# Kernel optimization log

Hardware: AMD Instinct MI355X
Metric: run time of the kernel (lower is better)

The kernel has to match this reference:

```python
import jax, jax.numpy as jnp
import numpy as np
from jax import lax

B, C, OUT, K, L = 8, 256, 256, 7, 2048
STRIDE, PAD, DIL = 1, 3, 1

def setup_inputs() -> dict:
    key = jax.random.key(0)
    k1, k2, k3, k4, k5 = jax.random.split(key, 5)
    return {
        "x": jax.random.normal(k1, (B, C, L), jnp.float32),
        "w_off": jax.random.normal(k2, (C * K * 2, C, K), jnp.float32) * 0.02,
        "b_off": jax.random.normal(k3, (C * K * 2,), jnp.float32) * 0.02,
        "weight": jax.random.normal(k4, (OUT, C, K), jnp.float32) * 0.02,
        "bias": jax.random.normal(k5, (OUT,), jnp.float32) * 0.02,
    }

def _gather_lin(x, idx):
    # x: (B,C,Lin), idx: (B,C,K,Lout) -> zero-padded gather along length
    Lin = x.shape[-1]
    valid = (idx >= 0) & (idx < Lin)
    idxc = jnp.clip(idx, 0, Lin - 1)
    v = jnp.take_along_axis(x[:, :, None, :], idxc, axis=3)
    return jnp.where(valid, v, jnp.zeros((), x.dtype))

def reference(x, w_off, b_off, weight, bias):
    # offset/mask predictor conv (same geometry as main conv)
    off = lax.conv_general_dilated(
        x, w_off, window_strides=(STRIDE,), padding=[(PAD, PAD)],
        rhs_dilation=(DIL,), dimension_numbers=("NCH", "OIH", "NCH"))
    off = off + b_off[None, :, None]
    Lout = off.shape[-1]
    off = off.reshape(B, 2, C * K, Lout)
    offset = off[:, 0].reshape(B, C, K, Lout)          # fractional shift per (c,k,p)
    mask = jax.nn.sigmoid(off[:, 1]).reshape(B, C, K, Lout)
    # base sampling grid: p*stride - pad + k*dil
    base = (jnp.arange(Lout) * STRIDE - PAD)[None, :] + (jnp.arange(K) * DIL)[:, None]  # (K,Lout)
    pos = offset + base[None, None].astype(x.dtype)    # (B,C,K,Lout)
    p0 = jnp.floor(pos)
    frac = pos - p0
    p0i = p0.astype(jnp.int32)
    sampled = _gather_lin(x, p0i) * (1.0 - frac) + _gather_lin(x, p0i + 1) * frac
    sampled = sampled * mask
    # grouped conv accumulate (groups=1): (B,C,K,L) x (O,C,K) -> (B,O,L)
    out = jnp.einsum("bckl,ock->bol", sampled, weight) + bias[None, :, None]
    return out
```

## Files before the change

### kernel.cpp

```cpp
#include <hip/hip_runtime.h>

typedef unsigned short ushort_t;
typedef __attribute__((ext_vector_type(8))) short bf16x8;
typedef __attribute__((ext_vector_type(4))) float f32x4;

constexpr int BB   = 8;
constexpr int CC   = 256;
constexpr int OUTC = 256;
constexpr int KK   = 7;
constexpr int LL   = 2048;
constexpr int PADc = 3;
constexpr int KD   = CC * KK;
constexpr int MOFF = CC * KK * 2;
constexpr int NTOT = BB * LL;
constexpr int NKSTEPS = KD / 32;
constexpr int LP   = LL + 6;

__device__ __forceinline__ ushort_t f2bf(float f) {
    unsigned u = __float_as_uint(f);
    unsigned r = (u + 0x7fffu + ((u >> 16) & 1u)) >> 16;
    return (ushort_t)r;
}

__global__ __launch_bounds__(256) void cast_k(const float4* __restrict__ src,
                                              ushort_t* __restrict__ dst, int n4) {
    int i = blockIdx.x * 256 + threadIdx.x;
    if (i >= n4) return;
    float4 v = src[i];
    ushort4 o;
    o.x = f2bf(v.x); o.y = f2bf(v.y); o.z = f2bf(v.z); o.w = f2bf(v.w);
    *(ushort4*)(dst + (size_t)i * 4) = o;
}

__global__ __launch_bounds__(256) void castperm_woff(const float* __restrict__ src,
                                                     ushort_t* __restrict__ dst) {
    int i = blockIdx.x * 256 + threadIdx.x;
    if (i >= MOFF * KD) return;
    int dr  = i / KD;
    int rem = i - dr * KD;
    int kk = rem >> 8, c = rem & 255;
    int r = (dr & 1) ? (KD + (dr >> 1)) : (dr >> 1);
    dst[i] = f2bf(src[(r * 256 + c) * 7 + kk]);
}

__global__ __launch_bounds__(256) void xpose_k(const float* __restrict__ x,
                                               ushort_t* __restrict__ xp) {
    __shared__ float tile[32][257];
    int bid = blockIdx.x;
    int b  = bid >> 6;
    int l0 = ((bid >> 3) & 7) * 256;
    int c0 = (bid & 7) * 32;
    int tid = threadIdx.x;
    const float* xb = x + (size_t)b * (CC * LL);
    ushort_t* xpb = xp + (size_t)b * (LP * 256);
#pragma unroll 4
    for (int k = 0; k < 32; ++k)
        tile[k][tid] = xb[(size_t)(c0 + k) * LL + l0 + tid];
    __syncthreads();
    int lp = l0 + tid + 3;
#pragma unroll
    for (int q = 0; q < 8; ++q) {
        ushort4 v;
        v.x = f2bf(tile[4 * q + 0][tid]);
        v.y = f2bf(tile[4 * q + 1][tid]);
        v.z = f2bf(tile[4 * q + 2][tid]);
        v.w = f2bf(tile[4 * q + 3][tid]);
        *(ushort4*)(xpb + (size_t)lp * 256 + c0 + 4 * q) = v;
    }
    if ((bid & 63) == 0) {
#pragma unroll
        for (int r = 0; r < 6; ++r) {
            int glp = (r < 3) ? r : (2048 + r);
            xpb[glp * 256 + tid] = 0;
        }
    }
}

__device__ __forceinline__ void load_lds16(const ushort_t* g, ushort_t* l) {
    __builtin_amdgcn_global_load_lds(
        (const __attribute__((address_space(1))) unsigned int*)g,
        (__attribute__((address_space(3))) unsigned int*)l, 16, 0, 0);
}

__device__ __forceinline__ void stage256A(ushort_t* ldsbuf,
                                          const ushort_t* __restrict__ A,
                                          int m0, int kt, int wid, int lane) {
    int t = wid * 64 + lane;
    int g = (t & 3) ^ ((t >> 3) & 3);
#pragma unroll
    for (int j = 0; j < 2; ++j) {
        int row = j * 128 + (t >> 2);
        load_lds16(A + (size_t)(m0 + row) * KD + kt * 32 + g * 8,
                   ldsbuf + j * 4096 + wid * 512);
    }
}
__device__ __forceinline__ void stage256B(ushort_t* ldsbuf,
                                          const ushort_t* __restrict__ xp,
                                          int n0, int kt, int wid, int lane) {
    int t = wid * 64 + lane;
    int g = (t & 3) ^ ((t >> 3) & 3);
    int tap = kt >> 3, cs = kt & 7;
    const ushort_t* base = xp + (size_t)(n0 >> 11) * (LP * 256)
                              + (size_t)((n0 & 2047) + tap) * 256 + cs * 32 + g * 8;
#pragma unroll
    for (int j = 0; j < 2; ++j) {
        int row = j * 128 + (t >> 2);
        load_lds16(base + (size_t)row * 256,
                   ldsbuf + 8192 + j * 4096 + wid * 512);
    }
}

template <int VMC>
__device__ __forceinline__ void kstep256(const ushort_t* __restrict__ A,
                                         const ushort_t* __restrict__ xp,
                                         ushort_t* lds, int m0, int n0, int kt,
                                         int wid, int lane, int wr, int wc,
                                         int r15, int u, f32x4 (&acc)[8][4]) {
    asm volatile("s_waitcnt vmcnt(%0)" :: "n"(VMC) : "memory");
    __builtin_amdgcn_s_barrier();
    const ushort_t* buf = lds + (size_t)(kt & 3) * 16384;
    const ushort_t* pa = buf + (wr * 128 + r15) * 32 + u * 8;
    const ushort_t* pb = buf + 8192 + (wc * 64 + r15) * 32 + u * 8;
    bf16x8 af[8], bq[4];
#pragma unroll
    for (int j = 0; j < 4; ++j) bq[j] = *(const bf16x8*)(pb + j * 512);
#pragma unroll
    for (int i = 0; i < 4; ++i) af[i] = *(const bf16x8*)(pa + i * 512);
    if (kt + 3 < NKSTEPS)
        stage256A(lds + (size_t)((kt + 3) & 3) * 16384, A, m0, kt + 3, wid, lane);
    __builtin_amdgcn_s_setprio(1);
#pragma unroll
    for (int i = 0; i < 4; ++i)
#pragma unroll
        for (int j = 0; j < 4; ++j)
            acc[i][j] = __builtin_amdgcn_mfma_f32_16x16x32_bf16(af[i], bq[j], acc[i][j], 0, 0, 0);
    __builtin_amdgcn_s_setprio(0);
#pragma unroll
    for (int i = 4; i < 8; ++i) af[i] = *(const bf16x8*)(pa + i * 512);
    if (kt + 3 < NKSTEPS)
        stage256B(lds + (size_t)((kt + 3) & 3) * 16384, xp, n0, kt + 3, wid, lane);
    __builtin_amdgcn_s_barrier();
    __builtin_amdgcn_s_setprio(1);
#pragma unroll
    for (int i = 4; i < 8; ++i)
#pragma unroll
        for (int j = 0; j < 4; ++j)
            acc[i][j] = __builtin_amdgcn_mfma_f32_16x16x32_bf16(af[i], bq[j], acc[i][j], 0, 0, 0);
    __builtin_amdgcn_s_setprio(0);
}

__global__ __launch_bounds__(512, 2) void gemm256_off_fused(const ushort_t* __restrict__ A,
                                                            const ushort_t* __restrict__ xp,
                                                            const float* __restrict__ boff,
                                                            const float* __restrict__ x,
                                                            ushort_t* __restrict__ s) {
    __shared__ __align__(16) ushort_t lds[4 * 16384];
    constexpr int NT = NTOT / 256;
    constexpr int NWG = (MOFF / 256) * NT;
    int bid = blockIdx.x;
    int wg = (bid & 7) * (NWG / 8) + (bid >> 3);
    int mt = wg / NT, nt = wg % NT;
    int m0 = mt * 256, n0 = nt * 256;
    int tid = threadIdx.x, wid = tid >> 6, lane = tid & 63;
    int wr = wid >> 2, wc = wid & 3;
    int r15 = lane & 15, kh = lane >> 4;
    int u = kh ^ ((r15 >> 1) & 3);

    f32x4 acc[8][4] = {};

    stage256A(lds,             A,  m0, 0, wid, lane);
    stage256B(lds,             xp, n0, 0, wid, lane);
    stage256A(lds + 16384,     A,  m0, 1, wid, lane);
    stage256B(lds + 16384,     xp, n0, 1, wid, lane);
    stage256A(lds + 2 * 16384, A,  m0, 2, wid, lane);
    stage256B(lds + 2 * 16384, xp, n0, 2, wid, lane);

    for (int kt = 0; kt < NKSTEPS - 2; ++kt)
        kstep256<8>(A, xp, lds, m0, n0, kt, wid, lane, wr, wc, r15, u, acc);
    kstep256<4>(A, xp, lds, m0, n0, NKSTEPS - 2, wid, lane, wr, wc, r15, u, acc);
    kstep256<0>(A, xp, lds, m0, n0, NKSTEPS - 1, wid, lane, wr, wc, r15, u, acc);

    __syncthreads();
    ushort_t* st = lds;
#pragma unroll
    for (int i = 0; i < 8; ++i) {
        int mloc = wr * 128 + i * 16 + kh * 4;
        int ckb  = (m0 + mloc) >> 1;
        int ckl  = mloc >> 1;
        float bo0 = boff[ckb],     bm0 = boff[KD + ckb];
        float bo1 = boff[ckb + 1], bm1 = boff[KD + ckb + 1];
        int c0 = ckb / 7,       kk0 = ckb - c0 * 7;
        int c1 = (ckb + 1) / 7, kk1 = (ckb + 1) - c1 * 7;
#pragma unroll
        for (int j = 0; j < 4; ++j) {
            int nl = wc * 64 + j * 16 + r15;
            int n = n0 + nl;
            int b = n >> 11, l = n & 2047;
            const float* xb_ = x + (size_t)b * (CC * LL);
            f32x4 v = acc[i][j];
            ushort2 o2;
#pragma unroll
            for (int p = 0; p < 2; ++p) {
                float offv = v[2 * p]     + (p ? bo1 : bo0);
                float mpre = v[2 * p + 1] + (p ? bm1 : bm0);
                int c = p ? c1 : c0, kk = p ? kk1 : kk0;
                float mask = 1.0f / (1.0f + __expf(-mpre));
                float pos = offv + (float)(l - PADc + kk);
                float p0f = floorf(pos);
                float frac = pos - p0f;
                int p0 = (int)p0f;
                const float* xr = xb_ + (size_t)c * LL;
                float x0 = ((unsigned)p0 < (unsigned)LL) ? xr[p0] : 0.0f;
                float x1 = ((unsigned)(p0 + 1) < (unsigned)LL) ? xr[p0 + 1] : 0.0f;
                float sv = (x0 + (x1 - x0) * frac) * mask;
                if (p) o2.y = f2bf(sv); else o2.x = f2bf(sv);
            }
            *(ushort2*)(st + nl * 136 + ckl) = o2;
        }
    }
    __syncthreads();
    int srow = tid >> 5;
    int scol = tid & 31;
    int ck0g = m0 >> 1;
#pragma unroll
    for (int pass = 0; pass < 16; ++pass) {
        int nl = pass * 16 + srow;
        ushort4 v4 = *(const ushort4*)(st + nl * 136 + scol * 4);
        *(ushort4*)(s + (size_t)(n0 + nl) * KD + ck0g + scol * 4) = v4;
    }
}

__device__ __forceinline__ void stage128(ushort_t* ldsbuf,
                                         const ushort_t* __restrict__ A,
                                         const ushort_t* __restrict__ Bt,
                                         int m0, int n0, int kt,
                                         int wid, int lane) {
    int t = wid * 64 + lane;
    int g = (t & 3) ^ ((t >> 3) & 3);
#pragma unroll
    for (int j = 0; j < 2; ++j) {
        int row = j * 64 + (t >> 2);
        load_lds16(A  + (size_t)(m0 + row) * KD + kt * 32 + g * 8,
                   ldsbuf + j * 2048 + wid * 512);
        load_lds16(Bt + (size_t)(n0 + row) * KD + kt * 32 + g * 8,
                   ldsbuf + 4096 + j * 2048 + wid * 512);
    }
}

template <int VMC>
__device__ __forceinline__ void kstep128(const ushort_t* __restrict__ A,
                                         const ushort_t* __restrict__ Bt,
                                         ushort_t* lds, int m0, int n0, int kt,
                                         int wid, int lane, int wr, int wc,
                                         int r15, int u, f32x4 (&acc)[4][4]) {
    asm volatile("s_waitcnt vmcnt(%0)" :: "n"(VMC) : "memory");
    __builtin_amdgcn_s_barrier();
    const ushort_t* buf = lds + (size_t)(kt & 3) * 8192;
    const ushort_t* pa = buf + (wr * 64 + r15) * 32 + u * 8;
    const ushort_t* pb = buf + 4096 + (wc * 64 + r15) * 32 + u * 8;
    bf16x8 af[4], bq[4];
#pragma unroll
    for (int i = 0; i < 4; ++i) af[i] = *(const bf16x8*)(pa + i * 512);
#pragma unroll
    for (int j = 0; j < 4; ++j) bq[j] = *(const bf16x8*)(pb + j * 512);
    if (kt + 3 < NKSTEPS)
        stage128(lds + (size_t)((kt + 3) & 3) * 8192, A, Bt, m0, n0, kt + 3, wid, lane);
    __builtin_amdgcn_s_setprio(1);
#pragma unroll
    for (int i = 0; i < 4; ++i)
#pragma unroll
        for (int j = 0; j < 4; ++j)
            acc[i][j] = __builtin_amdgcn_mfma_f32_16x16x32_bf16(af[i], bq[j], acc[i][j], 0, 0, 0);
    __builtin_amdgcn_s_setprio(0);
}

__global__ __launch_bounds__(256, 2) void gemm128_out(const ushort_t* __restrict__ A,
                                                      const ushort_t* __restrict__ Bt,
                                                      const float* __restrict__ bvec,
                                                      float* __restrict__ Dout) {
    __shared__ __align__(16) ushort_t lds[4 * 8192];
    constexpr int NT = NTOT / 128;
    constexpr int NWG = (OUTC / 128) * NT;
    int bid = blockIdx.x;
    int wg = (bid & 7) * (NWG / 8) + (bid >> 3);
    int mt = wg / NT, nt = wg % NT;
    int m0 = mt * 128, n0 = nt * 128;
    int tid = threadIdx.x, wid = tid >> 6, lane = tid & 63;
    int wr = wid >> 1, wc = wid & 1;
    int r15 = lane & 15, kh = lane >> 4;
    int u = kh ^ ((r15 >> 1) & 3);

    f32x4 acc[4][4] = {};

    stage128(lds,            A, Bt, m0, n0, 0, wid, lane);
    stage128(lds + 8192,     A, Bt, m0, n0, 1, wid, lane);
    stage128(lds + 2 * 8192, A, Bt, m0, n0, 2, wid, lane);

    for (int kt = 0; kt < NKSTEPS - 2; ++kt)
        kstep128<8>(A, Bt, lds, m0, n0, kt, wid, lane, wr, wc, r15, u, acc);
    kstep128<4>(A, Bt, lds, m0, n0, NKSTEPS - 2, wid, lane, wr, wc, r15, u, acc);
    kstep128<0>(A, Bt, lds, m0, n0, NKSTEPS - 1, wid, lane, wr, wc, r15, u, acc);

    int rbase = kh * 4;
#pragma unroll
    for (int i = 0; i < 4; ++i)
#pragma unroll
        for (int j = 0; j < 4; ++j) {
            int m = m0 + wr * 64 + i * 16 + rbase;
            int n = n0 + wc * 64 + j * 16 + r15;
            int b = n >> 11, l = n & 2047;
#pragma unroll
            for (int r = 0; r < 4; ++r) {
                float val = acc[i][j][r] + bvec[m + r];
                Dout[((size_t)(b * OUTC + (m + r))) * LL + l] = val;
            }
        }
}

extern "C" void kernel_launch(void* const* d_in, const int* in_sizes, int n_in,
                              void* d_out, int out_size, void* d_ws, size_t ws_size,
                              hipStream_t stream) {
    const float* x      = (const float*)d_in[0];
    const float* w_off  = (const float*)d_in[1];
    const float* b_off  = (const float*)d_in[2];
    const float* weight = (const float*)d_in[3];
    const float* bias   = (const float*)d_in[4];
    float* out = (float*)d_out;

    ushort_t* w = (ushort_t*)d_ws;
    ushort_t* wb  = w;
    ushort_t* wtb = wb  + MOFF * KD;
    ushort_t* xp  = wtb + OUTC * KD;
    ushort_t* s   = xp  + BB * LP * 256;

    castperm_woff<<<(MOFF * KD + 255) / 256, 256, 0, stream>>>(w_off, wb);
    cast_k<<<(114688 + 255) / 256, 256, 0, stream>>>((const float4*)weight, wtb, 114688);
    xpose_k<<<512, 256, 0, stream>>>(x, xp);

    gemm256_off_fused<<<(MOFF / 256) * (NTOT / 256), 512, 0, stream>>>(wb, xp, b_off, x, s);

    gemm128_out<<<(OUTC / 128) * (NTOT / 128), 256, 0, stream>>>(wtb, s, bias, out);
}
```

Baseline: 307.0 us.

## Restructure offset GEMM main loop into 64-wide K steps with quadrant ping-pong

Replaces the 4-stage 32-wide K pipeline with a double-buffered 64-wide K step. Each step splits the 256x256 tile into four 128x128 quadrants and computes them in turn, prefetching the next step's A/B halves between quadrant computations. The LDS layout changes to 64-element rows with an 8-way XOR swizzle. The epilogue index mapping is updated to the new warp-to-tile assignment. The intent is to cut barriers per K and overlap global loads with MFMA at finer grain, at the cost of more barriers per step and a shallower prefetch distance.

```diff
diff --git a/kernel.cpp b/kernel.cpp
--- a/kernel.cpp
+++ b/kernel.cpp
@@ -14,6 +14,7 @@
 constexpr int MOFF = CC * KK * 2;
 constexpr int NTOT = BB * LL;
 constexpr int NKSTEPS = KD / 32;
+constexpr int NT64 = KD / 64;
 constexpr int LP   = LL + 6;
 
 __device__ __forceinline__ ushort_t f2bf(float f) {
@@ -82,71 +83,130 @@
         (__attribute__((address_space(3))) unsigned int*)l, 16, 0, 0);
 }
 
-__device__ __forceinline__ void stage256A(ushort_t* ldsbuf,
-                                          const ushort_t* __restrict__ A,
-                                          int m0, int kt, int wid, int lane) {
-    int t = wid * 64 + lane;
-    int g = (t & 3) ^ ((t >> 3) & 3);
+__device__ __forceinline__ void stageA64(ushort_t* dst, const ushort_t* __restrict__ A,
+                                         int m0, int h, int kt, int wid, int lane) {
+    int gs = (lane & 7) ^ ((lane >> 3) & 7);
 #pragma unroll
     for (int j = 0; j < 2; ++j) {
-        int row = j * 128 + (t >> 2);
-        load_lds16(A + (size_t)(m0 + row) * KD + kt * 32 + g * 8,
-                   ldsbuf + j * 4096 + wid * 512);
-    }
-}
-__device__ __forceinline__ void stage256B(ushort_t* ldsbuf,
-                                          const ushort_t* __restrict__ xp,
-                                          int n0, int kt, int wid, int lane) {
-    int t = wid * 64 + lane;
-    int g = (t & 3) ^ ((t >> 3) & 3);
-    int tap = kt >> 3, cs = kt & 7;
+        int row = j * 64 + wid * 8 + (lane >> 3);
+        load_lds16(A + (size_t)(m0 + h * 128 + row) * KD + kt * 64 + gs * 8,
+                   dst + j * 4096 + wid * 512);
+    }
+}
+__device__ __forceinline__ void stageB64(ushort_t* dst, const ushort_t* __restrict__ xp,
+                                         int n0, int h, int kt, int wid, int lane) {
+    int gs = (lane & 7) ^ ((lane >> 3) & 7);
+    int tap = kt >> 2, cs = kt & 3;
     const ushort_t* base = xp + (size_t)(n0 >> 11) * (LP * 256)
-                              + (size_t)((n0 & 2047) + tap) * 256 + cs * 32 + g * 8;
+                         + (size_t)((n0 & 2047) + h * 128 + tap) * 256 + cs * 64 + gs * 8;
 #pragma unroll
     for (int j = 0; j < 2; ++j) {
-        int row = j * 128 + (t >> 2);
-        load_lds16(base + (size_t)row * 256,
-                   ldsbuf + 8192 + j * 4096 + wid * 512);
-    }
-}
-
-template <int VMC>
-__device__ __forceinline__ void kstep256(const ushort_t* __restrict__ A,
-                                         const ushort_t* __restrict__ xp,
-                                         ushort_t* lds, int m0, int n0, int kt,
-                                         int wid, int lane, int wr, int wc,
-                                         int r15, int u, f32x4 (&acc)[8][4]) {
-    asm volatile("s_waitcnt vmcnt(%0)" :: "n"(VMC) : "memory");
-    __builtin_amdgcn_s_barrier();
-    const ushort_t* buf = lds + (size_t)(kt & 3) * 16384;
-    const ushort_t* pa = buf + (wr * 128 + r15) * 32 + u * 8;
-    const ushort_t* pb = buf + 8192 + (wc * 64 + r15) * 32 + u * 8;
-    bf16x8 af[8], bq[4];
-#pragma unroll
-    for (int j = 0; j < 4; ++j) bq[j] = *(const bf16x8*)(pb + j * 512);
-#pragma unroll
-    for (int i = 0; i < 4; ++i) af[i] = *(const bf16x8*)(pa + i * 512);
-    if (kt + 3 < NKSTEPS)
-        stage256A(lds + (size_t)((kt + 3) & 3) * 16384, A, m0, kt + 3, wid, lane);
+        int row = j * 64 + wid * 8 + (lane >> 3);
+        load_lds16(base + (size_t)row * 256, dst + j * 4096 + wid * 512);
+    }
+}
+__device__ __forceinline__ bf16x8 rd64(const ushort_t* region, int rowbase,
+                                       int r15, int q, int kh, int l7) {
+    int u = (q * 4 + kh) ^ l7;
+    return *(const bf16x8*)(region + (rowbase + r15) * 64 + u * 8);
+}
+
+template <bool PF>
+__device__ __forceinline__ void kstep64(const ushort_t* __restrict__ A,
+                                        const ushort_t* __restrict__ xp,
+                                        ushort_t* lds, int m0, int n0, int t,
+                                        int wid, int lane, int wr, int wc,
+                                        int r15, int kh, int l7, f32x4 (&acc)[8][4]) {
+    const ushort_t* buf = lds + (t & 1) * 32768;
+    ushort_t* nbuf = lds + ((t + 1) & 1) * 32768;
+    const ushort_t* A0r = buf;
+    const ushort_t* A1r = buf + 8192;
+    const ushort_t* B0r = buf + 16384;
+    const ushort_t* B1r = buf + 24576;
+    bf16x8 af0[4][2], af1[4][2], bq0[2][2], bq1[2][2];
+#pragma unroll
+    for (int i = 0; i < 4; ++i) {
+        af0[i][0] = rd64(A0r, wr * 64 + i * 16, r15, 0, kh, l7);
+        af0[i][1] = rd64(A0r, wr * 64 + i * 16, r15, 1, kh, l7);
+    }
+#pragma unroll
+    for (int j = 0; j < 2; ++j) {
+        bq0[j][0] = rd64(B0r, wc * 32 + j * 16, r15, 0, kh, l7);
+        bq0[j][1] = rd64(B0r, wc * 32 + j * 16, r15, 1, kh, l7);
+    }
+    if (PF) {
+        stageA64(nbuf, A, m0, 0, t + 1, wid, lane);
+        stageB64(nbuf + 16384, xp, n0, 0, t + 1, wid, lane);
+        asm volatile("s_waitcnt vmcnt(6)" ::: "memory");
+    } else {
+        asm volatile("s_waitcnt vmcnt(0)" ::: "memory");
+    }
+    __builtin_amdgcn_s_barrier();
+    asm volatile("s_waitcnt lgkmcnt(0)" ::: "memory");
     __builtin_amdgcn_s_setprio(1);
 #pragma unroll
     for (int i = 0; i < 4; ++i)
 #pragma unroll
-        for (int j = 0; j < 4; ++j)
-            acc[i][j] = __builtin_amdgcn_mfma_f32_16x16x32_bf16(af[i], bq[j], acc[i][j], 0, 0, 0);
+        for (int j = 0; j < 2; ++j) {
+            acc[i][j] = __builtin_amdgcn_mfma_f32_16x16x32_bf16(af0[i][0], bq0[j][0], acc[i][j], 0, 0, 0);
+            acc[i][j] = __builtin_amdgcn_mfma_f32_16x16x32_bf16(af0[i][1], bq0[j][1], acc[i][j], 0, 0, 0);
+        }
     __builtin_amdgcn_s_setprio(0);
-#pragma unroll
-    for (int i = 4; i < 8; ++i) af[i] = *(const bf16x8*)(pa + i * 512);
-    if (kt + 3 < NKSTEPS)
-        stage256B(lds + (size_t)((kt + 3) & 3) * 16384, xp, n0, kt + 3, wid, lane);
-    __builtin_amdgcn_s_barrier();
+    __builtin_amdgcn_s_barrier();
+#pragma unroll
+    for (int j = 0; j < 2; ++j) {
+        bq1[j][0] = rd64(B1r, wc * 32 + j * 16, r15, 0, kh, l7);
+        bq1[j][1] = rd64(B1r, wc * 32 + j * 16, r15, 1, kh, l7);
+    }
+    if (PF) {
+        stageB64(nbuf + 24576, xp, n0, 1, t + 1, wid, lane);
+        asm volatile("s_waitcnt vmcnt(6)" ::: "memory");
+    }
+    __builtin_amdgcn_s_barrier();
+    asm volatile("s_waitcnt lgkmcnt(0)" ::: "memory");
     __builtin_amdgcn_s_setprio(1);
 #pragma unroll
-    for (int i = 4; i < 8; ++i)
-#pragma unroll
-        for (int j = 0; j < 4; ++j)
-            acc[i][j] = __builtin_amdgcn_mfma_f32_16x16x32_bf16(af[i], bq[j], acc[i][j], 0, 0, 0);
+    for (int i = 0; i < 4; ++i)
+#pragma unroll
+        for (int j = 0; j < 2; ++j) {
+            acc[i][j + 2] = __builtin_amdgcn_mfma_f32_16x16x32_bf16(af0[i][0], bq1[j][0], acc[i][j + 2], 0, 0, 0);
+            acc[i][j + 2] = __builtin_amdgcn_mfma_f32_16x16x32_bf16(af0[i][1], bq1[j][1], acc[i][j + 2], 0, 0, 0);
+        }
     __builtin_amdgcn_s_setprio(0);
+    __builtin_amdgcn_s_barrier();
+#pragma unroll
+    for (int i = 0; i < 4; ++i) {
+        af1[i][0] = rd64(A1r, wr * 64 + i * 16, r15, 0, kh, l7);
+        af1[i][1] = rd64(A1r, wr * 64 + i * 16, r15, 1, kh, l7);
+    }
+    if (PF) {
+        stageA64(nbuf + 8192, A, m0, 1, t + 1, wid, lane);
+        asm volatile("s_waitcnt vmcnt(6)" ::: "memory");
+    }
+    __builtin_amdgcn_s_barrier();
+    asm volatile("s_waitcnt lgkmcnt(0)" ::: "memory");
+    __builtin_amdgcn_s_setprio(1);
+#pragma unroll
+    for (int i = 0; i < 4; ++i)
+#pragma unroll
+        for (int j = 0; j < 2; ++j) {
+            acc[i + 4][j + 2] = __builtin_amdgcn_mfma_f32_16x16x32_bf16(af1[i][0], bq1[j][0], acc[i + 4][j + 2], 0, 0, 0);
+            acc[i + 4][j + 2] = __builtin_amdgcn_mfma_f32_16x16x32_bf16(af1[i][1], bq1[j][1], acc[i + 4][j + 2], 0, 0, 0);
+        }
+    __builtin_amdgcn_s_setprio(0);
+    __builtin_amdgcn_s_barrier();
+    if (PF) asm volatile("s_waitcnt vmcnt(4)" ::: "memory");
+    __builtin_amdgcn_s_barrier();
+    __builtin_amdgcn_s_setprio(1);
+#pragma unroll
+    for (int i = 0; i < 4; ++i)
+#pragma unroll
+        for (int j = 0; j < 2; ++j) {
+            acc[i + 4][j] = __builtin_amdgcn_mfma_f32_16x16x32_bf16(af1[i][0], bq0[j][0], acc[i + 4][j], 0, 0, 0);
+            acc[i + 4][j] = __builtin_amdgcn_mfma_f32_16x16x32_bf16(af1[i][1], bq0[j][1], acc[i + 4][j], 0, 0, 0);
+        }
+    __builtin_amdgcn_s_setprio(0);
+    __builtin_amdgcn_s_barrier();
 }
 
 __global__ __launch_bounds__(512, 2) void gemm256_off_fused(const ushort_t* __restrict__ A,
@@ -154,7 +214,7 @@
                                                             const float* __restrict__ boff,
                                                             const float* __restrict__ x,
                                                             ushort_t* __restrict__ s) {
-    __shared__ __align__(16) ushort_t lds[4 * 16384];
+    __shared__ __align__(16) ushort_t lds[2 * 32768];
     constexpr int NT = NTOT / 256;
     constexpr int NWG = (MOFF / 256) * NT;
     int bid = blockIdx.x;
@@ -163,28 +223,26 @@
     int m0 = mt * 256, n0 = nt * 256;
     int tid = threadIdx.x, wid = tid >> 6, lane = tid & 63;
     int wr = wid >> 2, wc = wid & 3;
-    int r15 = lane & 15, kh = lane >> 4;
-    int u = kh ^ ((r15 >> 1) & 3);
+    int r15 = lane & 15, kh = lane >> 4, l7 = lane & 7;
 
     f32x4 acc[8][4] = {};
 
-    stage256A(lds,             A,  m0, 0, wid, lane);
-    stage256B(lds,             xp, n0, 0, wid, lane);
-    stage256A(lds + 16384,     A,  m0, 1, wid, lane);
-    stage256B(lds + 16384,     xp, n0, 1, wid, lane);
-    stage256A(lds + 2 * 16384, A,  m0, 2, wid, lane);
-    stage256B(lds + 2 * 16384, xp, n0, 2, wid, lane);
-
-    for (int kt = 0; kt < NKSTEPS - 2; ++kt)
-        kstep256<8>(A, xp, lds, m0, n0, kt, wid, lane, wr, wc, r15, u, acc);
-    kstep256<4>(A, xp, lds, m0, n0, NKSTEPS - 2, wid, lane, wr, wc, r15, u, acc);
-    kstep256<0>(A, xp, lds, m0, n0, NKSTEPS - 1, wid, lane, wr, wc, r15, u, acc);
+    stageA64(lds,         A,  m0, 0, 0, wid, lane);
+    stageA64(lds + 8192,  A,  m0, 1, 0, wid, lane);
+    stageB64(lds + 16384, xp, n0, 0, 0, wid, lane);
+    stageB64(lds + 24576, xp, n0, 1, 0, wid, lane);
+    asm volatile("s_waitcnt vmcnt(0)" ::: "memory");
+    __builtin_amdgcn_s_barrier();
+
+    for (int t = 0; t < NT64 - 1; ++t)
+        kstep64<true>(A, xp, lds, m0, n0, t, wid, lane, wr, wc, r15, kh, l7, acc);
+    kstep64<false>(A, xp, lds, m0, n0, NT64 - 1, wid, lane, wr, wc, r15, kh, l7, acc);
 
     __syncthreads();
     ushort_t* st = lds;
 #pragma unroll
     for (int i = 0; i < 8; ++i) {
-        int mloc = wr * 128 + i * 16 + kh * 4;
+        int mloc = (i >> 2) * 128 + wr * 64 + (i & 3) * 16 + kh * 4;
         int ckb  = (m0 + mloc) >> 1;
         int ckl  = mloc >> 1;
         float bo0 = boff[ckb],     bm0 = boff[KD + ckb];
@@ -193,7 +251,7 @@
         int c1 = (ckb + 1) / 7, kk1 = (ckb + 1) - c1 * 7;
 #pragma unroll
         for (int j = 0; j < 4; ++j) {
-            int nl = wc * 64 + j * 16 + r15;
+            int nl = (j >> 1) * 128 + wc * 32 + (j & 1) * 16 + r15;
             int n = n0 + nl;
             int b = n >> 11, l = n & 2047;
             const float* xb_ = x + (size_t)b * (CC * LL);
@@ -219,8 +277,7 @@
         }
     }
     __syncthreads();
-    int srow = tid >> 5;
-    int scol = tid & 31;
+    int srow = tid >> 5, scol = tid & 31;
     int ck0g = m0 >> 1;
 #pragma unroll
     for (int pass = 0; pass < 16; ++pass) {
```

Measured after the change: 311.9 us. No clear change (+1.6%).
